# Optimization experiments

Hardware: AMD Instinct MI355X
Metric: run time of the kernel (lower is better)

## Reference

```python
import jax, jax.numpy as jnp
import numpy as np

N = 65536   # query points
M = 65536   # support points
H = 32      # neighbors per query
IN = 64     # input feature dim
OUT = 64    # out_dim // 2
K = 15      # kernel points
EXTENT = 0.1 * 1.2 / 2.5  # radius * kp_extent / conv_radius = 0.048
BN_EPS = 1e-5


def setup_inputs() -> dict:
    key = jax.random.key(0)
    ks = jax.random.split(key, 8)
    x = jax.random.normal(ks[0], (M, IN), dtype=jnp.float32)
    q_pts = jax.random.uniform(ks[1], (N, 3), dtype=jnp.float32) * 0.1
    s_pts = jax.random.uniform(ks[2], (M, 3), dtype=jnp.float32) * 0.1
    neighb_inds = jax.random.randint(ks[3], (N, H), 0, M, dtype=jnp.int32)
    kernel_points = jax.random.normal(ks[4], (K, 3), dtype=jnp.float32) * (0.5 * EXTENT)
    weights = jax.random.normal(ks[5], (K, IN, OUT), dtype=jnp.float32) * 0.05
    gamma = jnp.ones((OUT,), dtype=jnp.float32)
    beta = jnp.zeros((OUT,), dtype=jnp.float32)
    return {"x": x, "q_pts": q_pts, "s_pts": s_pts, "neighb_inds": neighb_inds,
            "kernel_points": kernel_points, "weights": weights,
            "gamma": gamma, "beta": beta}


def reference(x, q_pts, s_pts, neighb_inds, kernel_points, weights, gamma, beta):
    # --- KPConv (rigid, linear influence, sum aggregation) ---
    # Shadow point/feature for out-of-range neighbor indices (KPConv convention).
    s_pad = jnp.concatenate([s_pts, jnp.full((1, 3), 1e6, s_pts.dtype)], axis=0)
    x_pad = jnp.concatenate([x, jnp.zeros((1, x.shape[1]), x.dtype)], axis=0)

    # Relative neighbor coordinates: [N, H, 3]
    neighbors = s_pad[neighb_inds] - q_pts[:, None, :]
    # Squared distance to each kernel point: [N, H, K]
    diffs = neighbors[:, :, None, :] - kernel_points[None, None, :, :]
    sq_dist = jnp.sum(diffs * diffs, axis=-1)
    # Linear kernel-point influence, clipped at 0: [N, H, K]
    all_weights = jnp.maximum(1.0 - jnp.sqrt(sq_dist) / EXTENT, 0.0)

    # Gather neighbor features: [N, H, IN]
    neighb_x = x_pad[neighb_inds]
    # Influence-weighted aggregation per kernel point: [N, K, IN]
    weighted = jnp.einsum('nhk,nhi->nki', all_weights, neighb_x)
    # Apply per-kernel-point weight matrices and sum over kernel points: [N, OUT]
    out = jnp.einsum('nki,kio->no', weighted, weights)

    # --- BatchNorm (training-mode statistics over points) ---
    mean = jnp.mean(out, axis=0)
    var = jnp.var(out, axis=0)
    out = (out - mean) / jnp.sqrt(var + BN_EPS) * gamma + beta

    # --- LeakyReLU(0.1) ---
    return jnp.where(out >= 0, out, 0.1 * out)
```

## Files before the change

### kernel.cpp

```cpp
#include <hip/hip_runtime.h>
#include <math.h>

#define NQ   65536
#define H    32
#define IN   64
#define OUTC 64
#define K    15
#define QB   16
#define S_XN 68
#define S_WT 36
#define AK   72
#define AROW 1076
#define INV_EXT (1.0f / 0.048f)

#define OFF_PSUM  131072
#define OFF_SCSH  (OFF_PSUM + 2097152)
#define OFF_XBF   (OFF_SCSH + 1024)
#define NEED_BF16 (OFF_XBF + (size_t)NQ * IN * 2)

typedef __attribute__((ext_vector_type(8))) short short8;
typedef __attribute__((ext_vector_type(4))) short short4v;
typedef __attribute__((ext_vector_type(4))) float float4v;

static __device__ __forceinline__ unsigned short f2bf(float f) {
    return (unsigned short)((__float_as_uint(f) + 0x8000u) >> 16);
}
static __device__ __forceinline__ unsigned pk2(float a, float b) {
    return (__float_as_uint(a) + 0x8000u) >> 16 |
           ((__float_as_uint(b) + 0x8000u) & 0xFFFF0000u);
}

__global__ __launch_bounds__(256) void prep_all(
    const float* __restrict__ W, const float* __restrict__ x,
    short* __restrict__ Bfrag, unsigned short* __restrict__ xbf, int do_x)
{
    const int b = blockIdx.x;
    if (b < 4096) {
        if (do_x) {
            const int t = b * 256 + threadIdx.x;
            const float4 v = ((const float4*)x)[t];
            uint2 p; p.x = pk2(v.x, v.y); p.y = pk2(v.z, v.w);
            ((uint2*)xbf)[t] = p;
        }
    } else {
        const int t2 = (b - 4096) * 256 + threadIdx.x;
        const int o  = t2 & 63;
        const int i  = (t2 >> 6) & 63;
        const int kq = t2 >> 12;
        const int t  = kq * 2 + (i >> 5);
        const int lane = ((i >> 3) & 3) * 16 + (o & 15);
        const int v  = o >> 4;
        const int j  = i & 7;
        Bfrag[((v * 30 + t) * 64 + lane) * 8 + j] = (short)f2bf(W[t2]);
    }
}

template<bool BFX>
__global__ __launch_bounds__(256, 4) void kpconv_mfma(
    const float* __restrict__ x, const unsigned short* __restrict__ xbf,
    const float* __restrict__ qp, const float* __restrict__ sp,
    const int* __restrict__ inds, const float* __restrict__ kp,
    const short* __restrict__ Bfrag, float* __restrict__ out_raw,
    float* __restrict__ psum)
{
    __shared__ __align__(16) short lds[17920];
    short* xn  = lds;
    short* wT  = lds + 8704;
    short* Awt = lds;

    const int tid  = threadIdx.x;
    const int lane = tid & 63;
    const int wv   = tid >> 6;
    const int quad = lane >> 4;
    const int ml   = lane & 15;
    const int q0   = blockIdx.x * QB;

    short* xn_own = xn + wv * (H * S_XN);

    short4v xv[8];
    float4  xf[8];
    {
        const int ibase = (q0 + wv * 4) * H;
#pragma unroll
        for (int j = 0; j < 8; ++j) {
            const int id = inds[ibase + j * 4 + quad];
            if (BFX) xv[j] = *(const short4v*)((const short*)xbf + id * IN + ml * 4);
            else     xf[j] = *(const float4*)(x + id * IN + ml * 4);
        }
    }

    for (int rep = 0; rep < 2; ++rep) {
        const int p = lane + rep * 64;
        const int qi = p >> 5, h = p & 31;
        const int qg = wv * 4 + qi;
        const int n = q0 + qg;
        const int id = inds[n * H + h];
        const float dx = sp[id * 3 + 0] - qp[n * 3 + 0];
        const float dy = sp[id * 3 + 1] - qp[n * 3 + 1];
        const float dz = sp[id * 3 + 2] - qp[n * 3 + 2];
#pragma unroll
        for (int k = 0; k < K; ++k) {
            const float ex = dx - kp[k * 3 + 0];
            const float ey = dy - kp[k * 3 + 1];
            const float ez = dz - kp[k * 3 + 2];
            const float sq = ex * ex + ey * ey + ez * ez;
            float wval = 1.0f - __builtin_amdgcn_sqrtf(sq) * INV_EXT;
            wval = wval > 0.0f ? wval : 0.0f;
            wT[(qg * 16 + k) * S_WT + h] = (short)f2bf(wval);
        }
        wT[(qg * 16 + K) * S_WT + h] = 0;
    }

    float4v frag[4][4];
#pragma unroll
    for (int qi = 0; qi < 4; ++qi)
#pragma unroll
        for (int v = 0; v < 4; ++v) frag[qi][v] = (float4v){0.f, 0.f, 0.f, 0.f};

    for (int qi = 0; qi < 4; ++qi) {
        const int qg = wv * 4 + qi;

#pragma unroll
        for (int j = 0; j < 8; ++j) {
            const int h = j * 4 + quad;
            if (BFX) {
                *(short4v*)&xn_own[h * S_XN + ml * 4] = xv[j];
            } else {
                short4v p;
                p[0] = (short)f2bf(xf[j].x); p[1] = (short)f2bf(xf[j].y);
                p[2] = (short)f2bf(xf[j].z); p[3] = (short)f2bf(xf[j].w);
                *(short4v*)&xn_own[h * S_XN + ml * 4] = p;
            }
        }

        if (qi < 3) {
            const int ibase = (q0 + qg + 1) * H;
#pragma unroll
            for (int j = 0; j < 8; ++j) {
                const int id = inds[ibase + j * 4 + quad];
                if (BFX) xv[j] = *(const short4v*)((const short*)xbf + id * IN + ml * 4);
                else     xf[j] = *(const float4*)(x + id * IN + ml * 4);
            }
        }

        const int arow = (qg * 16 + ml) * S_WT + quad * 8;
        const short4v alo = *(const short4v*)&wT[arow];
        const short4v ahi = *(const short4v*)&wT[arow + 4];
        short8 a;
#pragma unroll
        for (int e = 0; e < 4; ++e) { a[e] = alo[e]; a[e + 4] = ahi[e]; }

#pragma unroll
        for (int v = 0; v < 4; ++v) {
            short8 bb;
#pragma unroll
            for (int j = 0; j < 8; ++j)
                bb[j] = xn_own[(quad * 8 + j) * S_XN + v * 16 + ml];
            frag[qi][v] = __builtin_amdgcn_mfma_f32_16x16x32_bf16(a, bb, frag[qi][v], 0, 0, 0);
        }
    }

    __syncthreads();

#pragma unroll
    for (int qi = 0; qi < 4; ++qi) {
        const int qg = wv * 4 + qi;
#pragma unroll
        for (int v = 0; v < 4; ++v) {
#pragma unroll
            for (int r = 0; r < 4; ++r) {
                const int kq = quad * 4 + r;
                if (kq < K)
                    Awt[qg * AROW + kq * AK + v * 16 + ml] = (short)f2bf(frag[qi][v][r]);
            }
        }
    }
    __syncthreads();

    float4v acc = (float4v){0.f, 0.f, 0.f, 0.f};
    const short* bptr = Bfrag + (wv * 30) * 512 + lane * 8;
#pragma unroll 2
    for (int t = 0; t < 30; ++t) {
        const int abase = ml * AROW + (t >> 1) * AK + (t & 1) * 32 + quad * 8;
        const short4v alo = *(const short4v*)&Awt[abase];
        const short4v ahi = *(const short4v*)&Awt[abase + 4];
        short8 a;
#pragma unroll
        for (int e = 0; e < 4; ++e) { a[e] = alo[e]; a[e + 4] = ahi[e]; }
        const short8 bb = *(const short8*)(bptr + t * 512);
        acc = __builtin_amdgcn_mfma_f32_16x16x32_bf16(a, bb, acc, 0, 0, 0);
    }

    float s = 0.f, s2 = 0.f;
#pragma unroll
    for (int r = 0; r < 4; ++r) {
        const float v = acc[r];
        out_raw[(q0 + quad * 4 + r) * OUTC + wv * 16 + ml] = v;
        s += v; s2 += v * v;
    }
    s  += __shfl_xor(s, 16, 64);  s  += __shfl_xor(s, 32, 64);
    s2 += __shfl_xor(s2, 16, 64); s2 += __shfl_xor(s2, 32, 64);
    if (quad == 0) {
        const int c = wv * 16 + ml;
        psum[c * 4096 + blockIdx.x]          = s;
        psum[262144 + c * 4096 + blockIdx.x] = s2;
    }
}

__global__ __launch_bounds__(256) void bn_stats(
    const float* __restrict__ psum, const float* __restrict__ gamma,
    const float* __restrict__ beta, float* __restrict__ sc_sh)
{
    const int c = blockIdx.x;
    const int t = threadIdx.x;
    float s = 0.f, q = 0.f;
#pragma unroll
    for (int i = 0; i < 16; ++i) {
        s += psum[c * 4096 + t + i * 256];
        q += psum[262144 + c * 4096 + t + i * 256];
    }
    __shared__ float rs[4], rq[4];
#pragma unroll
    for (int off = 32; off; off >>= 1) {
        s += __shfl_down(s, off, 64);
        q += __shfl_down(q, off, 64);
    }
    if ((t & 63) == 0) { rs[t >> 6] = s; rq[t >> 6] = q; }
    __syncthreads();
    if (t == 0) {
        s = rs[0] + rs[1] + rs[2] + rs[3];
        q = rq[0] + rq[1] + rq[2] + rq[3];
        const float mean = s * (1.0f / (float)NQ);
        const float var  = q * (1.0f / (float)NQ) - mean * mean;
        const float scale = gamma[c] / sqrtf(var + 1e-5f);
        sc_sh[c]      = scale;
        sc_sh[64 + c] = beta[c] - mean * scale;
    }
}

__global__ __launch_bounds__(256) void bn_apply(
    float* __restrict__ out, const float* __restrict__ sc_sh)
{
    __shared__ float sc[64];
    __shared__ float sh[64];
    if (threadIdx.x < 64) {
        sc[threadIdx.x] = sc_sh[threadIdx.x];
        sh[threadIdx.x] = sc_sh[64 + threadIdx.x];
    }
    __syncthreads();
    const int idx = blockIdx.x * 256 + threadIdx.x;
#pragma unroll
    for (int it = 0; it < 4; ++it) {
        const int e = idx + it * 262144;
        float4 v = ((const float4*)out)[e];
        const int cg = (e & 15) * 4;
        float4 r;
        r.x = v.x * sc[cg + 0] + sh[cg + 0];
        r.y = v.y * sc[cg + 1] + sh[cg + 1];
        r.z = v.z * sc[cg + 2] + sh[cg + 2];
        r.w = v.w * sc[cg + 3] + sh[cg + 3];
        r.x = r.x >= 0.0f ? r.x : 0.1f * r.x;
        r.y = r.y >= 0.0f ? r.y : 0.1f * r.y;
        r.z = r.z >= 0.0f ? r.z : 0.1f * r.z;
        r.w = r.w >= 0.0f ? r.w : 0.1f * r.w;
        ((float4*)out)[e] = r;
    }
}

extern "C" void kernel_launch(void* const* d_in, const int* in_sizes, int n_in,
                              void* d_out, int out_size, void* d_ws, size_t ws_size,
                              hipStream_t stream)
{
    (void)in_sizes; (void)n_in; (void)out_size;
    const float* x     = (const float*)d_in[0];
    const float* qp    = (const float*)d_in[1];
    const float* sp    = (const float*)d_in[2];
    const int*   inds  = (const int*)d_in[3];
    const float* kp    = (const float*)d_in[4];
    const float* W     = (const float*)d_in[5];
    const float* gamma = (const float*)d_in[6];
    const float* beta  = (const float*)d_in[7];
    float* out = (float*)d_out;

    short*          Bfrag = (short*)d_ws;
    float*          psum  = (float*)((char*)d_ws + OFF_PSUM);
    float*          sc_sh = (float*)((char*)d_ws + OFF_SCSH);
    unsigned short* xbf   = (unsigned short*)((char*)d_ws + OFF_XBF);

    const int use_bf = (ws_size >= NEED_BF16) ? 1 : 0;

    prep_all<<<4336, 256, 0, stream>>>(W, x, Bfrag, xbf, use_bf);
    if (use_bf)
        kpconv_mfma<true><<<NQ / QB, 256, 0, stream>>>(x, xbf, qp, sp, inds, kp, Bfrag, out, psum);
    else
        kpconv_mfma<false><<<NQ / QB, 256, 0, stream>>>(x, xbf, qp, sp, inds, kp, Bfrag, out, psum);
    bn_stats<<<64, 256, 0, stream>>>(psum, gamma, beta, sc_sh);
    bn_apply<<<1024, 256, 0, stream>>>(out, sc_sh);
}
```

Baseline: 152.7 us.

## Gather neighbor features directly into MFMA B fragments, skip LDS staging

Replaces the LDS transpose of gathered neighbor features with per-lane gathers that load each element straight into the register layout the MFMA B operand expects, double-buffered across queries. This removes the LDS store, the strided LDS reads and a chunk of shared memory. The cost is many scalar 2-byte global loads in place of vectorized 8-byte loads, so memory transactions per gather go up. The second-stage weight fragment load is also software-prefetched one iteration ahead.

```diff
diff --git a/kernel.cpp b/kernel.cpp
--- a/kernel.cpp
+++ b/kernel.cpp
@@ -7,7 +7,6 @@
 #define OUTC 64
 #define K    15
 #define QB   16
-#define S_XN 68
 #define S_WT 36
 #define AK   72
 #define AROW 1076
@@ -63,9 +62,8 @@
     const short* __restrict__ Bfrag, float* __restrict__ out_raw,
     float* __restrict__ psum)
 {
-    __shared__ __align__(16) short lds[17920];
-    short* xn  = lds;
-    short* wT  = lds + 8704;
+    __shared__ __align__(16) short lds[17216];
+    short* wT  = lds;
     short* Awt = lds;
 
     const int tid  = threadIdx.x;
@@ -75,17 +73,15 @@
     const int ml   = lane & 15;
     const int q0   = blockIdx.x * QB;
 
-    short* xn_own = xn + wv * (H * S_XN);
-
-    short4v xv[8];
-    float4  xf[8];
-    {
-        const int ibase = (q0 + wv * 4) * H;
+    short8 g0[4], g1[4];
+    if (BFX) {
+        const int ib = (q0 + wv * 4) * H + quad * 8;
 #pragma unroll
         for (int j = 0; j < 8; ++j) {
-            const int id = inds[ibase + j * 4 + quad];
-            if (BFX) xv[j] = *(const short4v*)((const short*)xbf + id * IN + ml * 4);
-            else     xf[j] = *(const float4*)(x + id * IN + ml * 4);
+            const int id = inds[ib + j];
+            const unsigned short* p = xbf + id * IN + ml;
+#pragma unroll
+            for (int v = 0; v < 4; ++v) g0[v][j] = (short)p[v * 16];
         }
     }
 
@@ -117,29 +113,32 @@
 #pragma unroll
         for (int v = 0; v < 4; ++v) frag[qi][v] = (float4v){0.f, 0.f, 0.f, 0.f};
 
+#pragma unroll
     for (int qi = 0; qi < 4; ++qi) {
         const int qg = wv * 4 + qi;
 
-#pragma unroll
-        for (int j = 0; j < 8; ++j) {
-            const int h = j * 4 + quad;
-            if (BFX) {
-                *(short4v*)&xn_own[h * S_XN + ml * 4] = xv[j];
-            } else {
-                short4v p;
-                p[0] = (short)f2bf(xf[j].x); p[1] = (short)f2bf(xf[j].y);
-                p[2] = (short)f2bf(xf[j].z); p[3] = (short)f2bf(xf[j].w);
-                *(short4v*)&xn_own[h * S_XN + ml * 4] = p;
+        short8* cur = (qi & 1) ? g1 : g0;
+        short8* nxt = (qi & 1) ? g0 : g1;
+
+        if (BFX) {
+            if (qi < 3) {
+                const int ib = (q0 + qg + 1) * H + quad * 8;
+#pragma unroll
+                for (int j = 0; j < 8; ++j) {
+                    const int id = inds[ib + j];
+                    const unsigned short* p = xbf + id * IN + ml;
+#pragma unroll
+                    for (int v = 0; v < 4; ++v) nxt[v][j] = (short)p[v * 16];
+                }
             }
-        }
-
-        if (qi < 3) {
-            const int ibase = (q0 + qg + 1) * H;
+        } else {
+            const int ib = (q0 + qg) * H + quad * 8;
 #pragma unroll
             for (int j = 0; j < 8; ++j) {
-                const int id = inds[ibase + j * 4 + quad];
-                if (BFX) xv[j] = *(const short4v*)((const short*)xbf + id * IN + ml * 4);
-                else     xf[j] = *(const float4*)(x + id * IN + ml * 4);
+                const int id = inds[ib + j];
+                const float* p = x + id * IN + ml;
+#pragma unroll
+                for (int v = 0; v < 4; ++v) cur[v][j] = (short)f2bf(p[v * 16]);
             }
         }
 
@@ -151,13 +150,8 @@
         for (int e = 0; e < 4; ++e) { a[e] = alo[e]; a[e + 4] = ahi[e]; }
 
 #pragma unroll
-        for (int v = 0; v < 4; ++v) {
-            short8 bb;
-#pragma unroll
-            for (int j = 0; j < 8; ++j)
-                bb[j] = xn_own[(quad * 8 + j) * S_XN + v * 16 + ml];
-            frag[qi][v] = __builtin_amdgcn_mfma_f32_16x16x32_bf16(a, bb, frag[qi][v], 0, 0, 0);
-        }
+        for (int v = 0; v < 4; ++v)
+            frag[qi][v] = __builtin_amdgcn_mfma_f32_16x16x32_bf16(a, cur[v], frag[qi][v], 0, 0, 0);
     }
 
     __syncthreads();
@@ -179,16 +173,19 @@
 
     float4v acc = (float4v){0.f, 0.f, 0.f, 0.f};
     const short* bptr = Bfrag + (wv * 30) * 512 + lane * 8;
+    short8 bcur = *(const short8*)(bptr);
 #pragma unroll 2
     for (int t = 0; t < 30; ++t) {
+        short8 bnxt = bcur;
+        if (t < 29) bnxt = *(const short8*)(bptr + (t + 1) * 512);
         const int abase = ml * AROW + (t >> 1) * AK + (t & 1) * 32 + quad * 8;
         const short4v alo = *(const short4v*)&Awt[abase];
         const short4v ahi = *(const short4v*)&Awt[abase + 4];
         short8 a;
 #pragma unroll
         for (int e = 0; e < 4; ++e) { a[e] = alo[e]; a[e + 4] = ahi[e]; }
-        const short8 bb = *(const short8*)(bptr + t * 512);
-        acc = __builtin_amdgcn_mfma_f32_16x16x32_bf16(a, bb, acc, 0, 0, 0);
+        acc = __builtin_amdgcn_mfma_f32_16x16x32_bf16(a, bcur, acc, 0, 0, 0);
+        bcur = bnxt;
     }
 
     float s = 0.f, s2 = 0.f;
```

After: 170.1 us. +11.4%, slower.
